# Performance work log

Measured on AMD Instinct MI355X. Metric: run time of the kernel, lower is better.

Reference implementation:

```python
import jax, jax.numpy as jnp
import numpy as np

B, T, C = 4, 2048, 1024
WIN = 16


def setup_inputs() -> dict:
    key = jax.random.key(0)
    ks = jax.random.split(key, 5)
    s = 1.0 / np.sqrt(C)
    return {
        "x": jax.random.normal(ks[0], (B, T, C), dtype=jnp.float32),
        "Wq": jax.random.normal(ks[1], (C, C), dtype=jnp.float32) * s,
        "bq": jnp.zeros((C,), jnp.float32),
        "Wk": jax.random.normal(ks[2], (C, C), dtype=jnp.float32) * s,
        "bk": jnp.zeros((C,), jnp.float32),
        "Wv": jax.random.normal(ks[3], (C, C), dtype=jnp.float32) * s,
        "bv": jnp.zeros((C,), jnp.float32),
        "Wo": jax.random.normal(ks[4], (C, C), dtype=jnp.float32) * s,
        "bo": jnp.zeros((C,), jnp.float32),
        "window": WIN,
    }


def reference(x, Wq, bq, Wk, bk, Wv, bv, Wo, bo, window):
    Bn, Tn, Cn = x.shape
    half = window // 2
    W = 2 * half + 1  # keys per query (window [t-half, t+half])
    q = x @ Wq.T + bq
    k = x @ Wk.T + bk
    v = x @ Wv.T + bv
    offs = jnp.arange(-half, half + 1)              # [W]
    tpos = jnp.arange(Tn)                            # [T]
    idx = tpos[:, None] + offs[None, :]              # [T, W]
    valid = (idx >= 0) & (idx < Tn)                  # [T, W]
    idx_c = jnp.clip(idx, 0, Tn - 1)
    k_win = k[:, idx_c, :]                           # [B, T, W, C]
    v_win = v[:, idx_c, :]                           # [B, T, W, C]
    scale = 1.0 / jnp.sqrt(jnp.asarray(Cn, x.dtype))
    scores = jnp.einsum('btc,btwc->btw', q, k_win) * scale
    scores = jnp.where(valid[None, :, :], scores, jnp.finfo(x.dtype).min)
    attn = jax.nn.softmax(scores, axis=-1)           # [B, T, W]
    ctx = jnp.einsum('btw,btwc->btc', attn, v_win)   # [B, T, C]
    return ctx @ Wo.T + bo
```

## Files before the change

kernel.cpp:

```cpp
#include <hip/hip_runtime.h>
#include <cstdint>
#include <cstddef>

#define B_ 4
#define T_ 2048
#define C_ 1024
#define M_ (B_ * T_)
#define HALF_ 8
#define W_ 17
#define QKV_STRIDE 3072

typedef unsigned short u16;
typedef _Float16 half8 __attribute__((ext_vector_type(8)));
typedef _Float16 half2_t __attribute__((ext_vector_type(2)));
typedef float f32x4 __attribute__((ext_vector_type(4)));

__device__ __forceinline__ void gload_lds16(const u16* g, u16* l) {
#if __has_builtin(__builtin_amdgcn_global_load_lds)
    __builtin_amdgcn_global_load_lds(
        (const __attribute__((address_space(1))) void*)g,
        (__attribute__((address_space(3))) void*)l, 16, 0, 0);
#else
    *(uint4*)(l + (threadIdx.x & 63) * 8) = *(const uint4*)g;
#endif
}

__device__ __forceinline__ float dot16(half8 a, half8 b, float acc) {
#if __has_builtin(__builtin_amdgcn_fdot2)
    const half2_t* pa = (const half2_t*)&a;
    const half2_t* pb = (const half2_t*)&b;
#pragma unroll
    for (int e = 0; e < 4; ++e) acc = __builtin_amdgcn_fdot2(pa[e], pb[e], acc, false);
#else
#pragma unroll
    for (int e = 0; e < 8; ++e) acc += (float)a[e] * (float)b[e];
#endif
    return acc;
}

__global__ void prologue(const float* __restrict__ x,
                         const float* __restrict__ Wq, const float* __restrict__ Wk,
                         const float* __restrict__ Wv, const float* __restrict__ Wo,
                         const float* __restrict__ bq, const float* __restrict__ bk,
                         const float* __restrict__ bv,
                         u16* __restrict__ xh, u16* __restrict__ wcat,
                         u16* __restrict__ woh, float* __restrict__ bcat) {
    const int blk = blockIdx.x;
    if (blk >= 12288) {
        int i = (blk - 12288) * 256 + threadIdx.x;
        const float* src = (i < 1024) ? bq : (i < 2048) ? bk : bv;
        bcat[i] = src[i & 1023];
        return;
    }
    const float* src;
    u16* dst;
    int j;
    if (blk < 8192)       { src = x;  dst = xh;   j = blk * 256 + threadIdx.x; }
    else if (blk < 11264) {
        int bb = blk - 8192;
        int sel = bb >> 10;
        src = (sel == 0) ? Wq : (sel == 1) ? Wk : Wv;
        dst = wcat + ((size_t)sel << 20);
        j = (bb - (sel << 10)) * 256 + threadIdx.x;
    } else                { src = Wo; dst = woh;  j = (blk - 11264) * 256 + threadIdx.x; }
    float4 v = ((const float4*)src)[j];
    ushort4 o;
    _Float16 a = (_Float16)v.x; o.x = __builtin_bit_cast(unsigned short, a);
    _Float16 b = (_Float16)v.y; o.y = __builtin_bit_cast(unsigned short, b);
    _Float16 c = (_Float16)v.z; o.z = __builtin_bit_cast(unsigned short, c);
    _Float16 d = (_Float16)v.w; o.w = __builtin_bit_cast(unsigned short, d);
    ((ushort4*)dst)[j] = o;
}

template <int OUT_F16>
__global__ __launch_bounds__(256) void gemm_nt_lds(
    const u16* __restrict__ A, const u16* __restrict__ Bw,
    const float* __restrict__ bias, void* __restrict__ Cout,
    int Ndim, int Kdim)
{
    __shared__ __align__(16) u16 As[128 * 32];
    __shared__ __align__(16) u16 Bs[128 * 32];

    const int tid  = threadIdx.x;
    const int lane = tid & 63;
    const int wave = tid >> 6;
    const int m0 = blockIdx.y * 128;
    const int n0 = blockIdx.x * 128;
    const int wm = (wave >> 1) * 64;
    const int wn = (wave & 1) * 64;

    const int srow = wave * 32 + (lane >> 2);
    const int kc = ((lane & 3) ^ ((lane >> 3) & 3)) * 8;
    const u16* Ap = A  + (size_t)(m0 + srow) * Kdim + kc;
    const u16* Bp = Bw + (size_t)(n0 + srow) * Kdim + kc;
    const size_t skip16 = (size_t)16 * Kdim;
    u16* AsW = As + wave * 1024;
    u16* BsW = Bs + wave * 1024;

    f32x4 zero = {0.f, 0.f, 0.f, 0.f};
    f32x4 acc[4][4];
#pragma unroll
    for (int i = 0; i < 4; ++i)
#pragma unroll
        for (int j = 0; j < 4; ++j) acc[i][j] = zero;

    const int fr = lane & 15;
    const int fk = (((lane >> 4) ^ ((lane >> 1) & 3)) & 3) * 8;

    for (int k0 = 0; k0 < Kdim; k0 += 32) {
        __syncthreads();
        gload_lds16(Ap + k0,          AsW);
        gload_lds16(Ap + k0 + skip16, AsW + 512);
        gload_lds16(Bp + k0,          BsW);
        gload_lds16(Bp + k0 + skip16, BsW + 512);
        __syncthreads();

        half8 af[4], bf[4];
#pragma unroll
        for (int i = 0; i < 4; ++i)
            af[i] = *(const half8*)&As[(wm + i * 16 + fr) * 32 + fk];
#pragma unroll
        for (int j = 0; j < 4; ++j)
            bf[j] = *(const half8*)&Bs[(wn + j * 16 + fr) * 32 + fk];
#pragma unroll
        for (int i = 0; i < 4; ++i)
#pragma unroll
            for (int j = 0; j < 4; ++j)
                acc[i][j] = __builtin_amdgcn_mfma_f32_16x16x32_f16(af[i], bf[j], acc[i][j], 0, 0, 0);
    }

#pragma unroll
    for (int i = 0; i < 4; ++i) {
        const int row0 = m0 + wm + i * 16 + (lane >> 4) * 4;
#pragma unroll
        for (int j = 0; j < 4; ++j) {
            const int col = n0 + wn + j * 16 + (lane & 15);
            const float bv = bias[col];
#pragma unroll
            for (int r = 0; r < 4; ++r) {
                float val = acc[i][j][r] + bv;
                if (OUT_F16) {
                    _Float16 h = (_Float16)val;
                    ((u16*)Cout)[(size_t)(row0 + r) * Ndim + col] = __builtin_bit_cast(unsigned short, h);
                } else {
                    ((float*)Cout)[(size_t)(row0 + r) * Ndim + col] = val;
                }
            }
        }
    }
}

__global__ __launch_bounds__(256) void attn_local(
    const u16* __restrict__ qkv, u16* __restrict__ ctx)
{
    const int wid  = blockIdx.x * 4 + (threadIdx.x >> 6);
    const int lane = threadIdx.x & 63;
    const int b = wid >> 11;
    const int t = wid & (T_ - 1);
    const int base = b * T_;
    const size_t qrow = (size_t)(base + t) * QKV_STRIDE;
    const int c0 = lane * 8;

    half8 q0 = *(const half8*)(qkv + qrow + c0);
    half8 q1 = *(const half8*)(qkv + qrow + 512 + c0);

    float s[W_];
#pragma unroll
    for (int o = 0; o < W_; ++o) {
        int j = t - HALF_ + o;
        int jc = min(max(j, 0), T_ - 1);
        const size_t kb = (size_t)(base + jc) * QKV_STRIDE + 1024;
        half8 k0v = *(const half8*)(qkv + kb + c0);
        half8 k1v = *(const half8*)(qkv + kb + 512 + c0);
        float d = dot16(q1, k1v, dot16(q0, k0v, 0.f));
#pragma unroll
        for (int off = 32; off > 0; off >>= 1)
            d += __shfl_xor(d, off);
        s[o] = (j == jc) ? d * 0.03125f : -3.0e38f;
    }

    float mx = s[0];
#pragma unroll
    for (int o = 1; o < W_; ++o) mx = fmaxf(mx, s[o]);
    float den = 0.f;
#pragma unroll
    for (int o = 0; o < W_; ++o) den += __expf(s[o] - mx);
    const float inv = 1.f / den;

    float acc0[8], acc1[8];
#pragma unroll
    for (int e = 0; e < 8; ++e) { acc0[e] = 0.f; acc1[e] = 0.f; }
#pragma unroll
    for (int o = 0; o < W_; ++o) {
        int j = t - HALF_ + o;
        int jc = min(max(j, 0), T_ - 1);
        const float wt = __expf(s[o] - mx) * inv;
        const size_t vb_ = (size_t)(base + jc) * QKV_STRIDE + 2048;
        half8 v0 = *(const half8*)(qkv + vb_ + c0);
        half8 v1 = *(const half8*)(qkv + vb_ + 512 + c0);
#pragma unroll
        for (int e = 0; e < 8; ++e) {
            acc0[e] += wt * (float)v0[e];
            acc1[e] += wt * (float)v1[e];
        }
    }

    const size_t crow = (size_t)(base + t) * C_;
    half8 o0, o1;
#pragma unroll
    for (int e = 0; e < 8; ++e) { o0[e] = (_Float16)acc0[e]; o1[e] = (_Float16)acc1[e]; }
    *(half8*)(ctx + crow + c0) = o0;
    *(half8*)(ctx + crow + 512 + c0) = o1;
}

extern "C" void kernel_launch(void* const* d_in, const int* in_sizes, int n_in,
                              void* d_out, int out_size, void* d_ws, size_t ws_size,
                              hipStream_t stream) {
    const float* x  = (const float*)d_in[0];
    const float* Wq = (const float*)d_in[1];
    const float* bq = (const float*)d_in[2];
    const float* Wk = (const float*)d_in[3];
    const float* bk = (const float*)d_in[4];
    const float* Wv = (const float*)d_in[5];
    const float* bv = (const float*)d_in[6];
    const float* Wo = (const float*)d_in[7];
    const float* bo = (const float*)d_in[8];
    float* out = (float*)d_out;

    u16* xh   = (u16*)d_ws;
    u16* wcat = xh   + (size_t)M_ * C_;
    u16* woh  = wcat + (size_t)3 * C_ * C_;
    u16* qkvh = woh  + (size_t)C_ * C_;
    u16* ctxh = qkvh + (size_t)M_ * QKV_STRIDE;
    float* bcat = (float*)(ctxh + (size_t)M_ * C_);

    prologue<<<12300, 256, 0, stream>>>(x, Wq, Wk, Wv, Wo, bq, bk, bv,
                                        xh, wcat, woh, bcat);

    dim3 gqkv(QKV_STRIDE / 128, M_ / 128);
    gemm_nt_lds<1><<<gqkv, 256, 0, stream>>>(xh, wcat, bcat, qkvh, QKV_STRIDE, C_);

    attn_local<<<M_ / 4, 256, 0, stream>>>(qkvh, ctxh);

    dim3 go(C_ / 128, M_ / 128);
    gemm_nt_lds<0><<<go, 256, 0, stream>>>(ctxh, woh, bo, out, C_, C_);
}
```

Measured before the change: 247.1 us.

## Use 32x32 MFMA tiles in GEMM and process two queries per wave in attention

The GEMM inner loop moves from 16x16x32 MFMA fragments to 32x32x16 fragments with a matching LDS swizzle and epilogue index mapping. This cuts LDS fragment loads per MFMA and may raise MFMA throughput. The attention kernel now gives each wave two adjacent queries, sharing 18 K/V row loads instead of 17 per query, which roughly halves K/V global traffic. In exchange it uses more registers per thread and launches half as many blocks.

```diff
diff --git a/kernel.cpp b/kernel.cpp
--- a/kernel.cpp
+++ b/kernel.cpp
@@ -13,7 +13,7 @@
 typedef unsigned short u16;
 typedef _Float16 half8 __attribute__((ext_vector_type(8)));
 typedef _Float16 half2_t __attribute__((ext_vector_type(2)));
-typedef float f32x4 __attribute__((ext_vector_type(4)));
+typedef float f32x16 __attribute__((ext_vector_type(16)));
 
 __device__ __forceinline__ void gload_lds16(const u16* g, u16* l) {
 #if __has_builtin(__builtin_amdgcn_global_load_lds)
@@ -97,15 +97,17 @@
     u16* AsW = As + wave * 1024;
     u16* BsW = Bs + wave * 1024;
 
-    f32x4 zero = {0.f, 0.f, 0.f, 0.f};
-    f32x4 acc[4][4];
-#pragma unroll
-    for (int i = 0; i < 4; ++i)
-#pragma unroll
-        for (int j = 0; j < 4; ++j) acc[i][j] = zero;
-
-    const int fr = lane & 15;
-    const int fk = (((lane >> 4) ^ ((lane >> 1) & 3)) & 3) * 8;
+    f32x16 acc[2][2];
+#pragma unroll
+    for (int i = 0; i < 2; ++i)
+#pragma unroll
+        for (int j = 0; j < 2; ++j)
+#pragma unroll
+            for (int r = 0; r < 16; ++r) acc[i][j][r] = 0.f;
+
+    const int rr = lane & 31;
+    const int hi = lane >> 5;
+    const int sw = (lane >> 1) & 3;
 
     for (int k0 = 0; k0 < Kdim; k0 += 32) {
         __syncthreads();
@@ -115,35 +117,39 @@
         gload_lds16(Bp + k0 + skip16, BsW + 512);
         __syncthreads();
 
-        half8 af[4], bf[4];
-#pragma unroll
-        for (int i = 0; i < 4; ++i)
-            af[i] = *(const half8*)&As[(wm + i * 16 + fr) * 32 + fk];
-#pragma unroll
-        for (int j = 0; j < 4; ++j)
-            bf[j] = *(const half8*)&Bs[(wn + j * 16 + fr) * 32 + fk];
-#pragma unroll
-        for (int i = 0; i < 4; ++i)
-#pragma unroll
-            for (int j = 0; j < 4; ++j)
-                acc[i][j] = __builtin_amdgcn_mfma_f32_16x16x32_f16(af[i], bf[j], acc[i][j], 0, 0, 0);
-    }
-
-#pragma unroll
-    for (int i = 0; i < 4; ++i) {
-        const int row0 = m0 + wm + i * 16 + (lane >> 4) * 4;
-#pragma unroll
-        for (int j = 0; j < 4; ++j) {
-            const int col = n0 + wn + j * 16 + (lane & 15);
+#pragma unroll
+        for (int kk = 0; kk < 2; ++kk) {
+            const int slot = ((kk * 2 + hi) ^ sw) * 8;
+            half8 af[2], bf[2];
+#pragma unroll
+            for (int i = 0; i < 2; ++i)
+                af[i] = *(const half8*)&As[(wm + i * 32 + rr) * 32 + slot];
+#pragma unroll
+            for (int j = 0; j < 2; ++j)
+                bf[j] = *(const half8*)&Bs[(wn + j * 32 + rr) * 32 + slot];
+#pragma unroll
+            for (int i = 0; i < 2; ++i)
+#pragma unroll
+                for (int j = 0; j < 2; ++j)
+                    acc[i][j] = __builtin_amdgcn_mfma_f32_32x32x16_f16(af[i], bf[j], acc[i][j], 0, 0, 0);
+        }
+    }
+
+#pragma unroll
+    for (int i = 0; i < 2; ++i) {
+#pragma unroll
+        for (int j = 0; j < 2; ++j) {
+            const int col = n0 + wn + j * 32 + (lane & 31);
             const float bv = bias[col];
 #pragma unroll
-            for (int r = 0; r < 4; ++r) {
-                float val = acc[i][j][r] + bv;
+            for (int reg = 0; reg < 16; ++reg) {
+                const int row = m0 + wm + i * 32 + (reg & 3) + 8 * (reg >> 2) + 4 * (lane >> 5);
+                float val = acc[i][j][reg] + bv;
                 if (OUT_F16) {
                     _Float16 h = (_Float16)val;
-                    ((u16*)Cout)[(size_t)(row0 + r) * Ndim + col] = __builtin_bit_cast(unsigned short, h);
+                    ((u16*)Cout)[(size_t)row * Ndim + col] = __builtin_bit_cast(unsigned short, h);
                 } else {
-                    ((float*)Cout)[(size_t)(row0 + r) * Ndim + col] = val;
+                    ((float*)Cout)[(size_t)row * Ndim + col] = val;
                 }
             }
         }
@@ -155,62 +161,80 @@
 {
     const int wid  = blockIdx.x * 4 + (threadIdx.x >> 6);
     const int lane = threadIdx.x & 63;
-    const int b = wid >> 11;
-    const int t = wid & (T_ - 1);
+    const int b  = wid >> 10;
+    const int t0 = (wid & 1023) * 2;
     const int base = b * T_;
-    const size_t qrow = (size_t)(base + t) * QKV_STRIDE;
     const int c0 = lane * 8;
 
-    half8 q0 = *(const half8*)(qkv + qrow + c0);
-    half8 q1 = *(const half8*)(qkv + qrow + 512 + c0);
-
-    float s[W_];
-#pragma unroll
-    for (int o = 0; o < W_; ++o) {
-        int j = t - HALF_ + o;
+    const size_t q0row = (size_t)(base + t0) * QKV_STRIDE;
+    const size_t q1row = q0row + QKV_STRIDE;
+    half8 qa0 = *(const half8*)(qkv + q0row + c0);
+    half8 qa1 = *(const half8*)(qkv + q0row + 512 + c0);
+    half8 qb0 = *(const half8*)(qkv + q1row + c0);
+    half8 qb1 = *(const half8*)(qkv + q1row + 512 + c0);
+
+    float s0[W_], s1[W_];
+#pragma unroll
+    for (int r = 0; r < W_ + 1; ++r) {
+        int j  = t0 - HALF_ + r;
         int jc = min(max(j, 0), T_ - 1);
         const size_t kb = (size_t)(base + jc) * QKV_STRIDE + 1024;
-        half8 k0v = *(const half8*)(qkv + kb + c0);
-        half8 k1v = *(const half8*)(qkv + kb + 512 + c0);
-        float d = dot16(q1, k1v, dot16(q0, k0v, 0.f));
-#pragma unroll
-        for (int off = 32; off > 0; off >>= 1)
-            d += __shfl_xor(d, off);
-        s[o] = (j == jc) ? d * 0.03125f : -3.0e38f;
-    }
-
-    float mx = s[0];
-#pragma unroll
-    for (int o = 1; o < W_; ++o) mx = fmaxf(mx, s[o]);
-    float den = 0.f;
-#pragma unroll
-    for (int o = 0; o < W_; ++o) den += __expf(s[o] - mx);
-    const float inv = 1.f / den;
-
-    float acc0[8], acc1[8];
-#pragma unroll
-    for (int e = 0; e < 8; ++e) { acc0[e] = 0.f; acc1[e] = 0.f; }
-#pragma unroll
-    for (int o = 0; o < W_; ++o) {
-        int j = t - HALF_ + o;
+        half8 k0 = *(const half8*)(qkv + kb + c0);
+        half8 k1 = *(const half8*)(qkv + kb + 512 + c0);
+        float d0 = dot16(qa1, k1, dot16(qa0, k0, 0.f));
+        float d1 = dot16(qb1, k1, dot16(qb0, k0, 0.f));
+#pragma unroll
+        for (int off = 32; off > 0; off >>= 1) {
+            d0 += __shfl_xor(d0, off);
+            d1 += __shfl_xor(d1, off);
+        }
+        const bool ok = (j == jc);
+        if (r < W_)  s0[r]     = ok ? d0 * 0.03125f : -3.0e38f;
+        if (r >= 1)  s1[r - 1] = ok ? d1 * 0.03125f : -3.0e38f;
+    }
+
+    float mx0 = s0[0], mx1 = s1[0];
+#pragma unroll
+    for (int o = 1; o < W_; ++o) { mx0 = fmaxf(mx0, s0[o]); mx1 = fmaxf(mx1, s1[o]); }
+    float den0 = 0.f, den1 = 0.f;
+#pragma unroll
+    for (int o = 0; o < W_; ++o) { den0 += __expf(s0[o] - mx0); den1 += __expf(s1[o] - mx1); }
+    const float inv0 = 1.f / den0, inv1 = 1.f / den1;
+
+    float acc0[16], acc1[16];
+#pragma unroll
+    for (int e = 0; e < 16; ++e) { acc0[e] = 0.f; acc1[e] = 0.f; }
+
+#pragma unroll
+    for (int r = 0; r < W_ + 1; ++r) {
+        int j  = t0 - HALF_ + r;
         int jc = min(max(j, 0), T_ - 1);
-        const float wt = __expf(s[o] - mx) * inv;
+        const float w0 = (r < W_)  ? __expf(s0[r]     - mx0) * inv0 : 0.f;
+        const float w1 = (r >= 1)  ? __expf(s1[r - 1] - mx1) * inv1 : 0.f;
         const size_t vb_ = (size_t)(base + jc) * QKV_STRIDE + 2048;
         half8 v0 = *(const half8*)(qkv + vb_ + c0);
         half8 v1 = *(const half8*)(qkv + vb_ + 512 + c0);
 #pragma unroll
         for (int e = 0; e < 8; ++e) {
-            acc0[e] += wt * (float)v0[e];
-            acc1[e] += wt * (float)v1[e];
-        }
-    }
-
-    const size_t crow = (size_t)(base + t) * C_;
-    half8 o0, o1;
-#pragma unroll
-    for (int e = 0; e < 8; ++e) { o0[e] = (_Float16)acc0[e]; o1[e] = (_Float16)acc1[e]; }
-    *(half8*)(ctx + crow + c0) = o0;
-    *(half8*)(ctx + crow + 512 + c0) = o1;
+            acc0[e]     += w0 * (float)v0[e];
+            acc0[e + 8] += w0 * (float)v1[e];
+            acc1[e]     += w1 * (float)v0[e];
+            acc1[e + 8] += w1 * (float)v1[e];
+        }
+    }
+
+    const size_t c0row = (size_t)(base + t0) * C_;
+    const size_t c1row = c0row + C_;
+    half8 o0, o1, o2, o3;
+#pragma unroll
+    for (int e = 0; e < 8; ++e) {
+        o0[e] = (_Float16)acc0[e];  o1[e] = (_Float16)acc0[e + 8];
+        o2[e] = (_Float16)acc1[e];  o3[e] = (_Float16)acc1[e + 8];
+    }
+    *(half8*)(ctx + c0row + c0) = o0;
+    *(half8*)(ctx + c0row + 512 + c0) = o1;
+    *(half8*)(ctx + c1row + c0) = o2;
+    *(half8*)(ctx + c1row + 512 + c0) = o3;
 }
 
 extern "C" void kernel_launch(void* const* d_in, const int* in_sizes, int n_in,
@@ -240,7 +264,7 @@
     dim3 gqkv(QKV_STRIDE / 128, M_ / 128);
     gemm_nt_lds<1><<<gqkv, 256, 0, stream>>>(xh, wcat, bcat, qkvh, QKV_STRIDE, C_);
 
-    attn_local<<<M_ / 4, 256, 0, stream>>>(qkvh, ctxh);
+    attn_local<<<M_ / 8, 256, 0, stream>>>(qkvh, ctxh);
 
     dim3 go(C_ / 128, M_ / 128);
     gemm_nt_lds<0><<<go, 256, 0, stream>>>(ctxh, woh, bo, out, C_, C_);
```

Result: faster. 232.8 us (-5.8%).

## Switch GEMMs to 32x32x16 MFMA and use 128x64 tiles for output projection

Applied to the files above, without the earlier changes.

Both GEMMs now use 32x32x16 f16 MFMA instructions instead of 16x16x32, giving each wave 2x2 (or 2x1) larger accumulator tiles and fewer LDS fragment reads per MFMA. The output projection gets a separate kernel with a 128x64 block tile, doubling its grid from 512 to 1024 blocks so more CUs are busy on the smaller N=1024 GEMM. The trade-off is more epilogue stores per lane with strided row patterns and reloading the A tile more often in the output GEMM.

```diff
diff --git a/kernel.cpp b/kernel.cpp
--- a/kernel.cpp
+++ b/kernel.cpp
@@ -13,7 +13,7 @@
 typedef unsigned short u16;
 typedef _Float16 half8 __attribute__((ext_vector_type(8)));
 typedef _Float16 half2_t __attribute__((ext_vector_type(2)));
-typedef float f32x4 __attribute__((ext_vector_type(4)));
+typedef float f32x16 __attribute__((ext_vector_type(16)));
 
 __device__ __forceinline__ void gload_lds16(const u16* g, u16* l) {
 #if __has_builtin(__builtin_amdgcn_global_load_lds)
@@ -72,10 +72,9 @@
     ((ushort4*)dst)[j] = o;
 }
 
-template <int OUT_F16>
 __global__ __launch_bounds__(256) void gemm_nt_lds(
     const u16* __restrict__ A, const u16* __restrict__ Bw,
-    const float* __restrict__ bias, void* __restrict__ Cout,
+    const float* __restrict__ bias, u16* __restrict__ Cout,
     int Ndim, int Kdim)
 {
     __shared__ __align__(16) u16 As[128 * 32];
@@ -97,15 +96,17 @@
     u16* AsW = As + wave * 1024;
     u16* BsW = Bs + wave * 1024;
 
-    f32x4 zero = {0.f, 0.f, 0.f, 0.f};
-    f32x4 acc[4][4];
-#pragma unroll
-    for (int i = 0; i < 4; ++i)
-#pragma unroll
-        for (int j = 0; j < 4; ++j) acc[i][j] = zero;
-
-    const int fr = lane & 15;
-    const int fk = (((lane >> 4) ^ ((lane >> 1) & 3)) & 3) * 8;
+    f32x16 acc[2][2];
+#pragma unroll
+    for (int i = 0; i < 2; ++i)
+#pragma unroll
+        for (int j = 0; j < 2; ++j)
+#pragma unroll
+            for (int r = 0; r < 16; ++r) acc[i][j][r] = 0.f;
+
+    const int rr = lane & 31;
+    const int hi = lane >> 5;
+    const int sw = (lane >> 1) & 3;
 
     for (int k0 = 0; k0 < Kdim; k0 += 32) {
         __syncthreads();
@@ -115,37 +116,102 @@
         gload_lds16(Bp + k0 + skip16, BsW + 512);
         __syncthreads();
 
-        half8 af[4], bf[4];
-#pragma unroll
-        for (int i = 0; i < 4; ++i)
-            af[i] = *(const half8*)&As[(wm + i * 16 + fr) * 32 + fk];
-#pragma unroll
-        for (int j = 0; j < 4; ++j)
-            bf[j] = *(const half8*)&Bs[(wn + j * 16 + fr) * 32 + fk];
-#pragma unroll
-        for (int i = 0; i < 4; ++i)
-#pragma unroll
-            for (int j = 0; j < 4; ++j)
-                acc[i][j] = __builtin_amdgcn_mfma_f32_16x16x32_f16(af[i], bf[j], acc[i][j], 0, 0, 0);
-    }
-
-#pragma unroll
-    for (int i = 0; i < 4; ++i) {
-        const int row0 = m0 + wm + i * 16 + (lane >> 4) * 4;
-#pragma unroll
-        for (int j = 0; j < 4; ++j) {
-            const int col = n0 + wn + j * 16 + (lane & 15);
+#pragma unroll
+        for (int kk = 0; kk < 2; ++kk) {
+            const int slot = ((kk * 2 + hi) ^ sw) * 8;
+            half8 af[2], bf[2];
+#pragma unroll
+            for (int i = 0; i < 2; ++i)
+                af[i] = *(const half8*)&As[(wm + i * 32 + rr) * 32 + slot];
+#pragma unroll
+            for (int j = 0; j < 2; ++j)
+                bf[j] = *(const half8*)&Bs[(wn + j * 32 + rr) * 32 + slot];
+#pragma unroll
+            for (int i = 0; i < 2; ++i)
+#pragma unroll
+                for (int j = 0; j < 2; ++j)
+                    acc[i][j] = __builtin_amdgcn_mfma_f32_32x32x16_f16(af[i], bf[j], acc[i][j], 0, 0, 0);
+        }
+    }
+
+#pragma unroll
+    for (int i = 0; i < 2; ++i) {
+#pragma unroll
+        for (int j = 0; j < 2; ++j) {
+            const int col = n0 + wn + j * 32 + (lane & 31);
             const float bv = bias[col];
 #pragma unroll
-            for (int r = 0; r < 4; ++r) {
-                float val = acc[i][j][r] + bv;
-                if (OUT_F16) {
-                    _Float16 h = (_Float16)val;
-                    ((u16*)Cout)[(size_t)(row0 + r) * Ndim + col] = __builtin_bit_cast(unsigned short, h);
-                } else {
-                    ((float*)Cout)[(size_t)(row0 + r) * Ndim + col] = val;
-                }
+            for (int reg = 0; reg < 16; ++reg) {
+                const int row = m0 + wm + i * 32 + (reg & 3) + 8 * (reg >> 2) + 4 * (lane >> 5);
+                _Float16 h = (_Float16)(acc[i][j][reg] + bv);
+                Cout[(size_t)row * Ndim + col] = __builtin_bit_cast(unsigned short, h);
             }
+        }
+    }
+}
+
+__global__ __launch_bounds__(256) void gemm_nt_64(
+    const u16* __restrict__ A, const u16* __restrict__ Bw,
+    const float* __restrict__ bias, float* __restrict__ Cout,
+    int Ndim, int Kdim)
+{
+    __shared__ __align__(16) u16 As[128 * 32];
+    __shared__ __align__(16) u16 Bs[64 * 32];
+
+    const int tid  = threadIdx.x;
+    const int lane = tid & 63;
+    const int wave = tid >> 6;
+    const int m0 = blockIdx.y * 128;
+    const int n0 = blockIdx.x * 64;
+    const int wm = (wave >> 1) * 64;
+    const int wn = (wave & 1) * 32;
+
+    const int sArow = wave * 32 + (lane >> 2);
+    const int sBrow = wave * 16 + (lane >> 2);
+    const int kc = ((lane & 3) ^ ((lane >> 3) & 3)) * 8;
+    const u16* Ap = A  + (size_t)(m0 + sArow) * Kdim + kc;
+    const u16* Bp = Bw + (size_t)(n0 + sBrow) * Kdim + kc;
+    const size_t skip16 = (size_t)16 * Kdim;
+    u16* AsW = As + wave * 1024;
+    u16* BsW = Bs + wave * 512;
+
+    f32x16 acc[2];
+#pragma unroll
+    for (int i = 0; i < 2; ++i)
+#pragma unroll
+        for (int r = 0; r < 16; ++r) acc[i][r] = 0.f;
+
+    const int rr = lane & 31;
+    const int hi = lane >> 5;
+    const int sw = (lane >> 1) & 3;
+
+    for (int k0 = 0; k0 < Kdim; k0 += 32) {
+        __syncthreads();
+        gload_lds16(Ap + k0,          AsW);
+        gload_lds16(Ap + k0 + skip16, AsW + 512);
+        gload_lds16(Bp + k0,          BsW);
+        __syncthreads();
+
+#pragma unroll
+        for (int kk = 0; kk < 2; ++kk) {
+            const int slot = ((kk * 2 + hi) ^ sw) * 8;
+            half8 bf = *(const half8*)&Bs[(wn + rr) * 32 + slot];
+#pragma unroll
+            for (int i = 0; i < 2; ++i) {
+                half8 af = *(const half8*)&As[(wm + i * 32 + rr) * 32 + slot];
+                acc[i] = __builtin_amdgcn_mfma_f32_32x32x16_f16(af, bf, acc[i], 0, 0, 0);
+            }
+        }
+    }
+
+    const int col = n0 + wn + (lane & 31);
+    const float bv = bias[col];
+#pragma unroll
+    for (int i = 0; i < 2; ++i) {
+#pragma unroll
+        for (int reg = 0; reg < 16; ++reg) {
+            const int row = m0 + wm + i * 32 + (reg & 3) + 8 * (reg >> 2) + 4 * (lane >> 5);
+            Cout[(size_t)row * Ndim + col] = acc[i][reg] + bv;
         }
     }
 }
@@ -238,10 +304,10 @@
                                         xh, wcat, woh, bcat);
 
     dim3 gqkv(QKV_STRIDE / 128, M_ / 128);
-    gemm_nt_lds<1><<<gqkv, 256, 0, stream>>>(xh, wcat, bcat, qkvh, QKV_STRIDE, C_);
+    gemm_nt_lds<<<gqkv, 256, 0, stream>>>(xh, wcat, bcat, qkvh, QKV_STRIDE, C_);
 
     attn_local<<<M_ / 4, 256, 0, stream>>>(qkvh, ctxh);
 
-    dim3 go(C_ / 128, M_ / 128);
-    gemm_nt_lds<0><<<go, 256, 0, stream>>>(ctxh, woh, bo, out, C_, C_);
-}
+    dim3 go(C_ / 64, M_ / 128);
+    gemm_nt_64<<<go, 256, 0, stream>>>(ctxh, woh, bo, out, C_, C_);
+}
```

New measurement: 235.9 us. 4.5% less time.

## Prepack weights into MFMA fragment layout and restructure GEMM with register prefetch

Applied to the files above, without the earlier changes.

The prologue now writes the fp16 weights directly in a per-wave 32x16 MFMA fragment order, so the GEMM reads B operands straight from global memory without staging them in LDS. The GEMM switches to 32x32x16 MFMA tiles, stages a 128x128 A panel in XOR-swizzled LDS, and prefetches the next A panel into registers while computing the current one. This is meant to cut LDS traffic, barriers per K step and per-iteration overhead. The cost is higher register pressure, a larger LDS footprint per block, and uncached global B reads that may be less efficient than LDS reuse.

```diff
diff --git a/kernel.cpp b/kernel.cpp
--- a/kernel.cpp
+++ b/kernel.cpp
@@ -13,17 +13,7 @@
 typedef unsigned short u16;
 typedef _Float16 half8 __attribute__((ext_vector_type(8)));
 typedef _Float16 half2_t __attribute__((ext_vector_type(2)));
-typedef float f32x4 __attribute__((ext_vector_type(4)));
-
-__device__ __forceinline__ void gload_lds16(const u16* g, u16* l) {
-#if __has_builtin(__builtin_amdgcn_global_load_lds)
-    __builtin_amdgcn_global_load_lds(
-        (const __attribute__((address_space(1))) void*)g,
-        (__attribute__((address_space(3))) void*)l, 16, 0, 0);
-#else
-    *(uint4*)(l + (threadIdx.x & 63) * 8) = *(const uint4*)g;
-#endif
-}
+typedef float f32x16 __attribute__((ext_vector_type(16)));
 
 __device__ __forceinline__ float dot16(half8 a, half8 b, float acc) {
 #if __has_builtin(__builtin_amdgcn_fdot2)
@@ -36,6 +26,15 @@
     for (int e = 0; e < 8; ++e) acc += (float)a[e] * (float)b[e];
 #endif
     return acc;
+}
+
+__device__ __forceinline__ ushort4 cvt4(float4 v) {
+    ushort4 o;
+    _Float16 a = (_Float16)v.x; o.x = __builtin_bit_cast(unsigned short, a);
+    _Float16 b = (_Float16)v.y; o.y = __builtin_bit_cast(unsigned short, b);
+    _Float16 c = (_Float16)v.z; o.z = __builtin_bit_cast(unsigned short, c);
+    _Float16 d = (_Float16)v.w; o.w = __builtin_bit_cast(unsigned short, d);
+    return o;
 }
 
 __global__ void prologue(const float* __restrict__ x,
@@ -43,107 +42,127 @@
                          const float* __restrict__ Wv, const float* __restrict__ Wo,
                          const float* __restrict__ bq, const float* __restrict__ bk,
                          const float* __restrict__ bv,
-                         u16* __restrict__ xh, u16* __restrict__ wcat,
-                         u16* __restrict__ woh, float* __restrict__ bcat) {
+                         u16* __restrict__ xh, u16* __restrict__ wfq,
+                         u16* __restrict__ wfo, float* __restrict__ bcat) {
     const int blk = blockIdx.x;
-    if (blk >= 12288) {
-        int i = (blk - 12288) * 256 + threadIdx.x;
+    if (blk < 8192) {
+        int j = blk * 256 + threadIdx.x;
+        ((ushort4*)xh)[j] = cvt4(((const float4*)x)[j]);
+        return;
+    }
+    if (blk >= 10240) {
+        int i = (blk - 10240) * 256 + threadIdx.x;
         const float* src = (i < 1024) ? bq : (i < 2048) ? bk : bv;
         bcat[i] = src[i & 1023];
         return;
     }
+    int c = (blk - 8192) * 256 + threadIdx.x;
     const float* src;
     u16* dst;
-    int j;
-    if (blk < 8192)       { src = x;  dst = xh;   j = blk * 256 + threadIdx.x; }
-    else if (blk < 11264) {
-        int bb = blk - 8192;
-        int sel = bb >> 10;
-        src = (sel == 0) ? Wq : (sel == 1) ? Wk : Wv;
-        dst = wcat + ((size_t)sel << 20);
-        j = (bb - (sel << 10)) * 256 + threadIdx.x;
-    } else                { src = Wo; dst = woh;  j = (blk - 11264) * 256 + threadIdx.x; }
-    float4 v = ((const float4*)src)[j];
-    ushort4 o;
-    _Float16 a = (_Float16)v.x; o.x = __builtin_bit_cast(unsigned short, a);
-    _Float16 b = (_Float16)v.y; o.y = __builtin_bit_cast(unsigned short, b);
-    _Float16 c = (_Float16)v.z; o.z = __builtin_bit_cast(unsigned short, c);
-    _Float16 d = (_Float16)v.w; o.w = __builtin_bit_cast(unsigned short, d);
-    ((ushort4*)dst)[j] = o;
+    int cc;
+    if (c < 393216) {
+        int mat = c / 131072;
+        src = (mat == 0) ? Wq : (mat == 1) ? Wk : Wv;
+        dst = wfq;  cc = c;  c = c % 131072;
+    } else {
+        src = Wo;  dst = wfo;  cc = c - 393216;  c = cc;
+    }
+    const int nt_local = c >> 12;
+    const int ks   = (c >> 6) & 63;
+    const int lane = c & 63;
+    const int row = nt_local * 32 + (lane & 31);
+    const int col = ks * 16 + (lane >> 5) * 8;
+    const float4* s = (const float4*)(src + (size_t)row * C_ + col);
+    ushort4* d = (ushort4*)(dst + (size_t)cc * 8);
+    d[0] = cvt4(s[0]);
+    d[1] = cvt4(s[1]);
 }
 
 template <int OUT_F16>
-__global__ __launch_bounds__(256) void gemm_nt_lds(
-    const u16* __restrict__ A, const u16* __restrict__ Bw,
+__global__ __launch_bounds__(256) void gemm_panel(
+    const u16* __restrict__ A, const u16* __restrict__ Bfrag,
     const float* __restrict__ bias, void* __restrict__ Cout,
     int Ndim, int Kdim)
 {
-    __shared__ __align__(16) u16 As[128 * 32];
-    __shared__ __align__(16) u16 Bs[128 * 32];
+    __shared__ __align__(16) u16 As[128 * 128];
 
     const int tid  = threadIdx.x;
     const int lane = tid & 63;
     const int wave = tid >> 6;
     const int m0 = blockIdx.y * 128;
-    const int n0 = blockIdx.x * 128;
     const int wm = (wave >> 1) * 64;
-    const int wn = (wave & 1) * 64;
-
-    const int srow = wave * 32 + (lane >> 2);
-    const int kc = ((lane & 3) ^ ((lane >> 3) & 3)) * 8;
-    const u16* Ap = A  + (size_t)(m0 + srow) * Kdim + kc;
-    const u16* Bp = Bw + (size_t)(n0 + srow) * Kdim + kc;
-    const size_t skip16 = (size_t)16 * Kdim;
-    u16* AsW = As + wave * 1024;
-    u16* BsW = Bs + wave * 1024;
-
-    f32x4 zero = {0.f, 0.f, 0.f, 0.f};
-    f32x4 acc[4][4];
-#pragma unroll
-    for (int i = 0; i < 4; ++i)
-#pragma unroll
-        for (int j = 0; j < 4; ++j) acc[i][j] = zero;
-
-    const int fr = lane & 15;
-    const int fk = (((lane >> 4) ^ ((lane >> 1) & 3)) & 3) * 8;
-
-    for (int k0 = 0; k0 < Kdim; k0 += 32) {
+    const int wnt = blockIdx.x * 4 + (wave & 1) * 2;
+
+    const int srow = tid >> 4;
+    const int clog = (tid & 15) ^ srow;
+    const u16* Ast = A + (size_t)(m0 + srow) * Kdim + clog * 8;
+    const size_t pskip = (size_t)16 * Kdim;
+    uint4* AsW = (uint4*)As + tid;
+
+    const int nks = Kdim >> 4;
+    const u16* Bf0 = Bfrag + ((size_t)(wnt + 0) * nks) * 512 + lane * 8;
+    const u16* Bf1 = Bfrag + ((size_t)(wnt + 1) * nks) * 512 + lane * 8;
+
+    f32x16 acc[2][2];
+#pragma unroll
+    for (int i = 0; i < 2; ++i)
+#pragma unroll
+        for (int j = 0; j < 2; ++j)
+#pragma unroll
+            for (int r = 0; r < 16; ++r) acc[i][j][r] = 0.f;
+
+    const int rl = lane & 31;
+    const int hi = lane >> 5;
+    const int sx = lane & 15;
+
+    uint4 pf[8];
+#pragma unroll
+    for (int p = 0; p < 8; ++p)
+        pf[p] = *(const uint4*)(Ast + (size_t)p * pskip);
+
+    for (int k0 = 0; k0 < Kdim; k0 += 128) {
+        if (k0) __syncthreads();
+#pragma unroll
+        for (int p = 0; p < 8; ++p)
+            AsW[p * 256] = pf[p];
         __syncthreads();
-        gload_lds16(Ap + k0,          AsW);
-        gload_lds16(Ap + k0 + skip16, AsW + 512);
-        gload_lds16(Bp + k0,          BsW);
-        gload_lds16(Bp + k0 + skip16, BsW + 512);
-        __syncthreads();
-
-        half8 af[4], bf[4];
-#pragma unroll
-        for (int i = 0; i < 4; ++i)
-            af[i] = *(const half8*)&As[(wm + i * 16 + fr) * 32 + fk];
-#pragma unroll
-        for (int j = 0; j < 4; ++j)
-            bf[j] = *(const half8*)&Bs[(wn + j * 16 + fr) * 32 + fk];
-#pragma unroll
-        for (int i = 0; i < 4; ++i)
-#pragma unroll
-            for (int j = 0; j < 4; ++j)
-                acc[i][j] = __builtin_amdgcn_mfma_f32_16x16x32_f16(af[i], bf[j], acc[i][j], 0, 0, 0);
-    }
-
-#pragma unroll
-    for (int i = 0; i < 4; ++i) {
-        const int row0 = m0 + wm + i * 16 + (lane >> 4) * 4;
-#pragma unroll
-        for (int j = 0; j < 4; ++j) {
-            const int col = n0 + wn + j * 16 + (lane & 15);
+
+        if (k0 + 128 < Kdim) {
+#pragma unroll
+            for (int p = 0; p < 8; ++p)
+                pf[p] = *(const uint4*)(Ast + k0 + 128 + (size_t)p * pskip);
+        }
+
+        const int ksb = k0 >> 4;
+#pragma unroll
+        for (int ks = 0; ks < 8; ++ks) {
+            half8 b0 = *(const half8*)(Bf0 + (size_t)(ksb + ks) * 512);
+            half8 b1 = *(const half8*)(Bf1 + (size_t)(ksb + ks) * 512);
+            const int pch = (ks * 2 + hi) ^ sx;
+            half8 a0 = *(const half8*)&As[((wm + rl) * 16 + pch) * 8];
+            half8 a1 = *(const half8*)&As[((wm + 32 + rl) * 16 + pch) * 8];
+            acc[0][0] = __builtin_amdgcn_mfma_f32_32x32x16_f16(a0, b0, acc[0][0], 0, 0, 0);
+            acc[0][1] = __builtin_amdgcn_mfma_f32_32x32x16_f16(a0, b1, acc[0][1], 0, 0, 0);
+            acc[1][0] = __builtin_amdgcn_mfma_f32_32x32x16_f16(a1, b0, acc[1][0], 0, 0, 0);
+            acc[1][1] = __builtin_amdgcn_mfma_f32_32x32x16_f16(a1, b1, acc[1][1], 0, 0, 0);
+        }
+    }
+
+#pragma unroll
+    for (int i = 0; i < 2; ++i) {
+#pragma unroll
+        for (int j = 0; j < 2; ++j) {
+            const int col = (wnt + j) * 32 + (lane & 31);
             const float bv = bias[col];
 #pragma unroll
-            for (int r = 0; r < 4; ++r) {
-                float val = acc[i][j][r] + bv;
+            for (int reg = 0; reg < 16; ++reg) {
+                const int row = m0 + wm + i * 32 + (reg & 3) + 8 * (reg >> 2) + 4 * (lane >> 5);
+                float val = acc[i][j][reg] + bv;
                 if (OUT_F16) {
                     _Float16 h = (_Float16)val;
-                    ((u16*)Cout)[(size_t)(row0 + r) * Ndim + col] = __builtin_bit_cast(unsigned short, h);
+                    ((u16*)Cout)[(size_t)row * Ndim + col] = __builtin_bit_cast(unsigned short, h);
                 } else {
-                    ((float*)Cout)[(size_t)(row0 + r) * Ndim + col] = val;
+                    ((float*)Cout)[(size_t)row * Ndim + col] = val;
                 }
             }
         }
@@ -228,20 +247,20 @@
     float* out = (float*)d_out;
 
     u16* xh   = (u16*)d_ws;
-    u16* wcat = xh   + (size_t)M_ * C_;
-    u16* woh  = wcat + (size_t)3 * C_ * C_;
-    u16* qkvh = woh  + (size_t)C_ * C_;
+    u16* wfq  = xh   + (size_t)M_ * C_;
+    u16* wfo  = wfq  + (size_t)3 * C_ * C_;
+    u16* qkvh = wfo  + (size_t)C_ * C_;
     u16* ctxh = qkvh + (size_t)M_ * QKV_STRIDE;
     float* bcat = (float*)(ctxh + (size_t)M_ * C_);
 
-    prologue<<<12300, 256, 0, stream>>>(x, Wq, Wk, Wv, Wo, bq, bk, bv,
-                                        xh, wcat, woh, bcat);
+    prologue<<<10252, 256, 0, stream>>>(x, Wq, Wk, Wv, Wo, bq, bk, bv,
+                                        xh, wfq, wfo, bcat);
 
     dim3 gqkv(QKV_STRIDE / 128, M_ / 128);
-    gemm_nt_lds<1><<<gqkv, 256, 0, stream>>>(xh, wcat, bcat, qkvh, QKV_STRIDE, C_);
+    gemm_panel<1><<<gqkv, 256, 0, stream>>>(xh, wfq, bcat, qkvh, QKV_STRIDE, C_);
 
     attn_local<<<M_ / 4, 256, 0, stream>>>(qkvh, ctxh);
 
     dim3 go(C_ / 128, M_ / 128);
-    gemm_nt_lds<0><<<go, 256, 0, stream>>>(ctxh, woh, bo, out, C_, C_);
-}
+    gemm_panel<0><<<go, 256, 0, stream>>>(ctxh, wfo, bo, out, C_, C_);
+}
```

Measured after the change: 337.6 us. +36.6%, slower.
